# Optimization experiments

Hardware: AMD Instinct MI355X
Metric: run time of the kernel (lower is better)

Reference implementation:

```python
import jax, jax.numpy as jnp
import numpy as np

# static config (matches init_kwargs)
B, HID, NH, D = 1, 1024, 16, 64
T, Hh, W = 8, 32, 32
TT, TH, TW = 2, 8, 8            # tile sizes (numel 128)
WT, WH, WW = 6 // TT, 16 // TH, 16 // TW  # window in tiles: 3,2,2
NTT, NTH, NTW = T // TT, Hh // TH, W // TW  # 4,4,4
NTILE = NTT * NTH * NTW          # 64
TILE = TT * TH * TW              # 128
WK = WT * WH * WW                # 12 kv tiles per q tile
S = T * Hh * W


def _dim_window(nt, w):
    left = w // 2
    right = w // 2 + (w % 2) - 1
    center = jnp.clip(jnp.arange(nt), left, nt - 1 - right)
    return center[:, None] - left + jnp.arange(w)  # [nt, w]


def _kv_tile_idx():
    kt = _dim_window(NTT, WT)  # [NTT, WT]
    kh = _dim_window(NTH, WH)  # [NTH, WH]
    kw = _dim_window(NTW, WW)  # [NTW, WW]
    idx = (kt[:, None, None, :, None, None] * (NTH * NTW)
           + kh[None, :, None, None, :, None] * NTW
           + kw[None, None, :, None, None, :])
    return idx.reshape(NTILE, WK)


def _to_tiles(x, nh):
    # [B, S, nh*D] -> [B, nh, NTILE, TILE, D]; seq laid out (ntt tt nth th ntw tw)
    x = x.reshape(B, NTT, TT, NTH, TH, NTW, TW, nh, D)
    x = x.transpose(0, 7, 1, 3, 5, 2, 4, 6, 8)
    return x.reshape(B, nh, NTILE, TILE, D)


def _from_tiles(o):
    # [B, NH, NTILE, TILE, D] -> [B, S, NH*D]
    o = o.reshape(B, NH, NTT, NTH, NTW, TT, TH, TW, D)
    o = o.transpose(0, 2, 5, 3, 6, 4, 7, 1, 8)
    return o.reshape(B, S, NH * D)


def setup_inputs() -> dict:
    key = jax.random.key(0)
    ks = jax.random.split(key, 5)
    sc = 1.0 / np.sqrt(HID)
    return {
        'hidden_states': jax.random.normal(ks[0], (B, S, HID), jnp.float32),
        'wq': jax.random.normal(ks[1], (HID, NH * D), jnp.float32) * sc,
        'wk': jax.random.normal(ks[2], (HID, NH * D), jnp.float32) * sc,
        'wv': jax.random.normal(ks[3], (HID, NH * D), jnp.float32) * sc,
        'wo': jax.random.normal(ks[4], (NH * D, HID), jnp.float32) * sc,
    }


def reference(hidden_states, wq, wk, wv, wo):
    kv_idx = _kv_tile_idx()  # [NTILE, WK]
    q = _to_tiles(hidden_states @ wq, NH)  # [B,NH,NTILE,TILE,D]
    k = _to_tiles(hidden_states @ wk, NH)
    v = _to_tiles(hidden_states @ wv, NH)
    # gather each query tile's exact kv window (mask fully satisfied by construction)
    kg = k[:, :, kv_idx].reshape(B, NH, NTILE, WK * TILE, D)
    vg = v[:, :, kv_idx].reshape(B, NH, NTILE, WK * TILE, D)
    scores = jnp.einsum('bhnqd,bhnkd->bhnqk', q, kg) * (1.0 / np.sqrt(D))
    p = jax.nn.softmax(scores, axis=-1)
    o = jnp.einsum('bhnqk,bhnkd->bhnqd', p, vg)
    return _from_tiles(o) @ wo
```

## Files before the change

kernel.cpp:

```cpp
#include <hip/hip_runtime.h>
#include <hip/hip_bf16.h>
#include <math.h>

typedef __attribute__((ext_vector_type(8))) short          short8;
typedef __attribute__((ext_vector_type(8))) unsigned short u16x8;
typedef __attribute__((ext_vector_type(2))) unsigned int   u32x2;
typedef __attribute__((ext_vector_type(4))) float          f32x4;

#define MFMA_BF16(a, b, c) __builtin_amdgcn_mfma_f32_16x16x32_bf16((a), (b), (c), 0, 0, 0)

#define GLOAD_LDS16(gp, lp)                                        \
  __builtin_amdgcn_global_load_lds(                                \
      (const __attribute__((address_space(1))) void*)(gp),         \
      (__attribute__((address_space(3))) void*)(lp), 16, 0, 0)


__device__ __forceinline__ unsigned short f2bf(float f) {
  union { float f; unsigned int u; } v; v.f = f;
  unsigned int r = v.u + 0x7fffu + ((v.u >> 16) & 1u);
  return (unsigned short)(r >> 16);
}
__device__ __forceinline__ unsigned int pack2bf(float a, float b) {
  union { float f; unsigned int u; } x, y; x.f = a; y.f = b;
  return ((x.u + 0x8000u) >> 16) | ((y.u + 0x8000u) & 0xffff0000u);
}

__device__ __forceinline__ int row_to_seq(int r) {
  int tile = r >> 7, pos = r & 127;
  int ntt = tile >> 4, nth = (tile >> 2) & 3, ntw = tile & 3;
  int tt  = pos >> 6,  th  = (pos >> 3) & 7,  tw  = pos & 7;
  return ((ntt * 2 + tt) << 10) | ((nth * 8 + th) << 5) | (ntw * 8 + tw);
}

__global__ __launch_bounds__(256) void permute_hs(const float* __restrict__ in,
                                                  unsigned short* __restrict__ out) {
  int cid = blockIdx.x * 256 + threadIdx.x;
  int r = cid >> 7, c = (cid & 127) * 8;
  int s = row_to_seq(r);
  const float* f = in + (size_t)s * 1024 + c;
  u16x8 v;
#pragma unroll
  for (int j = 0; j < 8; ++j) v[j] = f2bf(f[j]);
  *(u16x8*)(out + (size_t)r * 1024 + c) = v;
}

__global__ __launch_bounds__(256) void transpose_w(const float* __restrict__ w0,
                                                   const float* __restrict__ w1,
                                                   const float* __restrict__ w2,
                                                   const float* __restrict__ w3,
                                                   unsigned short* __restrict__ out) {
  __shared__ unsigned short Lt[64 * 68];
  int m = blockIdx.y;
  const float* W = (m == 0) ? w0 : (m == 1) ? w1 : (m == 2) ? w2 : w3;
  unsigned short* O = out + (size_t)m * 1048576;
  int k0 = (blockIdx.x >> 4) * 64, n0 = (blockIdx.x & 15) * 64;
  int tid = threadIdx.x;
#pragma unroll
  for (int i = 0; i < 2; ++i) {
    int cid = i * 256 + tid;
    int kr = cid >> 3, c = cid & 7;
    const float* f = W + (size_t)(k0 + kr) * 1024 + n0 + c * 8;
#pragma unroll
    for (int j = 0; j < 8; ++j) Lt[(c * 8 + j) * 68 + kr] = f2bf(f[j]);
  }
  __syncthreads();
#pragma unroll
  for (int i = 0; i < 2; ++i) {
    int cid = i * 256 + tid;
    int nr = cid >> 3, c = cid & 7;
    u16x8 v;
#pragma unroll
    for (int j = 0; j < 8; ++j) v[j] = Lt[nr * 68 + c * 8 + j];
    *(u16x8*)(O + (size_t)(n0 + nr) * 1024 + k0 + c * 8) = v;
  }
}

template <int SCATTER, int OUT_F32>
__device__ __forceinline__ void gemm_bt_body(const unsigned short* __restrict__ A,
                                             const unsigned short* __restrict__ Bt,
                                             void* __restrict__ Cv,
                                             int row0, int col0, float scale) {
  __shared__ unsigned short As[128 * 64];
  __shared__ unsigned short Bs[128 * 64];
  const int tid  = threadIdx.x;
  const int lane = tid & 63, w = tid >> 6;
  const int quad = lane >> 4, lm = lane & 15;
  const int wr = (w >> 1) * 64, wc = (w & 1) * 64;
  f32x4 acc[4][4] = {};
  for (int kt = 0; kt < 16; ++kt) {
    const int k0 = kt * 64;
    __syncthreads();
#pragma unroll
    for (int i = 0; i < 4; ++i) {
      int cid = i * 256 + tid;
      int r = cid >> 3, c = cid & 7;
      int cg = c ^ (r & 7);
      int base = (i * 256 + (tid & 192)) * 8;
      GLOAD_LDS16(A  + (size_t)(row0 + r) * 1024 + k0 + cg * 8, As + base);
      GLOAD_LDS16(Bt + (size_t)(col0 + r) * 1024 + k0 + cg * 8, Bs + base);
    }
    __syncthreads();
#pragma unroll
    for (int kh = 0; kh < 2; ++kh) {
      short8 af[4], bf[4];
#pragma unroll
      for (int t = 0; t < 4; ++t) {
        int ca = (kh * 4 + quad) ^ (lm & 7);
        af[t] = *(const short8*)(As + (wr + t * 16 + lm) * 64 + ca * 8);
        bf[t] = *(const short8*)(Bs + (wc + t * 16 + lm) * 64 + ca * 8);
      }
#pragma unroll
      for (int rt = 0; rt < 4; ++rt)
#pragma unroll
        for (int ct = 0; ct < 4; ++ct)
          acc[rt][ct] = MFMA_BF16(af[rt], bf[ct], acc[rt][ct]);
    }
  }
#pragma unroll
  for (int rt = 0; rt < 4; ++rt)
#pragma unroll
    for (int ct = 0; ct < 4; ++ct)
#pragma unroll
      for (int g = 0; g < 4; ++g) {
        int R  = row0 + wr + rt * 16 + quad * 4 + g;
        int Cc = col0 + wc + ct * 16 + lm;
        int Rs = SCATTER ? row_to_seq(R) : R;
        float vv = acc[rt][ct][g] * scale;
        if (OUT_F32) ((float*)Cv)[(size_t)Rs * 1024 + Cc] = vv;
        else ((unsigned short*)Cv)[(size_t)Rs * 1024 + Cc] = f2bf(vv);
      }
}

__global__ __launch_bounds__(256) void gemm_qkv(const unsigned short* __restrict__ A,
                                                const unsigned short* __restrict__ Wt,
                                                unsigned short* __restrict__ QKV) {
  float scale = (blockIdx.z == 0) ? 0.18033688011112042f : 1.0f;
  gemm_bt_body<0, 0>(A, Wt + (size_t)blockIdx.z * 1048576,
                     QKV + (size_t)blockIdx.z * 8388608,
                     blockIdx.y * 128, blockIdx.x * 128, scale);
}

__global__ __launch_bounds__(256) void gemm_out(const unsigned short* __restrict__ A,
                                                const unsigned short* __restrict__ Wt,
                                                float* __restrict__ Cout) {
  gemm_bt_body<1, 1>(A, Wt, Cout, blockIdx.y * 128, blockIdx.x * 128, 1.0f);
}

__global__ __launch_bounds__(256) void transpose_v(const unsigned short* __restrict__ V,
                                                   unsigned short* __restrict__ Vt) {
  __shared__ unsigned short Lt[64 * 136];
  int kt = blockIdx.x, h = blockIdx.y, tid = threadIdx.x;
#pragma unroll
  for (int i = 0; i < 4; ++i) {
    int cid = i * 256 + tid;
    int r = cid >> 3, c = cid & 7;
    u16x8 v = *(const u16x8*)(V + (size_t)(kt * 128 + r) * 1024 + h * 64 + c * 8);
#pragma unroll
    for (int j = 0; j < 8; ++j) Lt[(c * 8 + j) * 136 + r] = v[j];
  }
  __syncthreads();
#pragma unroll
  for (int i = 0; i < 4; ++i) {
    int cid = i * 256 + tid;
    int d = cid >> 4, c = cid & 15;
    u16x8 v = *(const u16x8*)(Lt + d * 136 + c * 8);
    *(u16x8*)(Vt + (size_t)(h * 64 + d) * 8192 + kt * 128 + c * 8) = v;
  }
}

__global__ __launch_bounds__(512, 4) void attn(const unsigned short* __restrict__ Q,
                                               const unsigned short* __restrict__ K,
                                               const unsigned short* __restrict__ Vt,
                                               unsigned short* __restrict__ O) {
  __shared__ unsigned short Ks[128 * 64];
  __shared__ unsigned short Vs[64 * 128];
  __shared__ unsigned short Pb[8 * 16 * 64];

  const int tid  = threadIdx.x;
  const int lane = tid & 63, w = tid >> 6;
  const int quad = lane >> 4, lm = lane & 15;
  unsigned short* Pbw = Pb + w * 1024;

  const int h = blockIdx.x >> 6, qt = blockIdx.x & 63;
  const int ntt = qt >> 4, nth = (qt >> 2) & 3, ntw = qt & 3;
  const int kt0 = min(max(ntt, 1), 2) - 1;
  const int kh0 = min(max(nth, 1), 3) - 1;
  const int kw0 = min(max(ntw, 1), 3) - 1;

  short8 bq[2];
#pragma unroll
  for (int kh = 0; kh < 2; ++kh)
    bq[kh] = *(const short8*)(Q + (size_t)(qt * 128 + w * 16 + lm) * 1024
                                + h * 64 + kh * 32 + quad * 8);

  short8 ones8;
#pragma unroll
  for (int j = 0; j < 8; ++j) ones8[j] = (short)0x3F80;

  f32x4 o_acc[4] = {};
  f32x4 l_acc = {};

  {
    const int kvt0 = kt0 * 16 + kh0 * 4 + kw0;
#pragma unroll
    for (int i = 0; i < 2; ++i) {
      int cid = i * 512 + tid;
      int r = cid >> 3, c = cid & 7, cg = c ^ (r & 7);
      int base = (i * 512 + (tid & 448)) * 8;
      GLOAD_LDS16(K + (size_t)(kvt0 * 128 + r) * 1024 + h * 64 + cg * 8, Ks + base);
    }
  }
  __syncthreads();

  for (int it = 0; it < 12; ++it) {
    const int tt2 = it >> 2, hh2 = (it >> 1) & 1, ww2 = it & 1;
    const int kvt = (kt0 + tt2) * 16 + (kh0 + hh2) * 4 + (kw0 + ww2);

#pragma unroll
    for (int i = 0; i < 2; ++i) {
      int cid = i * 512 + tid;
      int d = cid >> 4, c = cid & 15, cg = c ^ (d & 7);
      int base = (i * 512 + (tid & 448)) * 8;
      GLOAD_LDS16(Vt + (size_t)(h * 64 + d) * 8192 + kvt * 128 + cg * 8, Vs + base);
    }

    f32x4 sa[8] = {};
#pragma unroll
    for (int kh = 0; kh < 2; ++kh) {
      short8 ak[8];
#pragma unroll
      for (int rt = 0; rt < 8; ++rt)
        ak[rt] = *(const short8*)(Ks + (rt * 16 + lm) * 64 + (((kh * 4 + quad) ^ (lm & 7)) * 8));
#pragma unroll
      for (int rt = 0; rt < 8; ++rt)
        sa[rt] = MFMA_BF16(ak[rt], bq[kh], sa[rt]);
    }

    u32x2 pk[8];
#pragma unroll
    for (int rt = 0; rt < 8; ++rt) {
      pk[rt][0] = pack2bf(exp2f(sa[rt][0]), exp2f(sa[rt][1]));
      pk[rt][1] = pack2bf(exp2f(sa[rt][2]), exp2f(sa[rt][3]));
    }

    __syncthreads();

    if (it < 11) {
      const int jt = it + 1;
      const int t2 = jt >> 2, h2 = (jt >> 1) & 1, w2 = jt & 1;
      const int kvn = (kt0 + t2) * 16 + (kh0 + h2) * 4 + (kw0 + w2);
#pragma unroll
      for (int i = 0; i < 2; ++i) {
        int cid = i * 512 + tid;
        int r = cid >> 3, c = cid & 7, cg = c ^ (r & 7);
        int base = (i * 512 + (tid & 448)) * 8;
        GLOAD_LDS16(K + (size_t)(kvn * 128 + r) * 1024 + h * 64 + cg * 8, Ks + base);
      }
    }

#pragma unroll
    for (int half = 0; half < 2; ++half) {
#pragma unroll
      for (int rt4 = 0; rt4 < 4; ++rt4) {
        *(u32x2*)(Pbw + lm * 64 + (((rt4 * 2 + (quad >> 1)) ^ (lm & 7)) * 8) + (quad & 1) * 4)
            = pk[half * 4 + rt4];
      }
#pragma unroll
      for (int ks2 = 0; ks2 < 2; ++ks2) {
        short8 ap = *(const short8*)(Pbw + lm * 64 + (((ks2 * 4 + quad) ^ (lm & 7)) * 8));
        l_acc = MFMA_BF16(ap, ones8, l_acc);
        const int ks = half * 2 + ks2;
#pragma unroll
        for (int nt = 0; nt < 4; ++nt) {
          short8 bv = *(const short8*)(Vs + (nt * 16 + lm) * 128 + (((ks * 4 + quad) ^ (lm & 7)) * 8));
          o_acc[nt] = MFMA_BF16(ap, bv, o_acc[nt]);
        }
      }
    }

    __syncthreads();
  }

#pragma unroll
  for (int g = 0; g < 4; ++g) {
    float inv = 1.0f / l_acc[g];
#pragma unroll
    for (int nt = 0; nt < 4; ++nt) {
      int R = qt * 128 + w * 16 + quad * 4 + g;
      O[(size_t)R * 1024 + h * 64 + nt * 16 + lm] = f2bf(o_acc[nt][g] * inv);
    }
  }
}

extern "C" void kernel_launch(void* const* d_in, const int* in_sizes, int n_in,
                              void* d_out, int out_size, void* d_ws, size_t ws_size,
                              hipStream_t stream) {
  const float* hs = (const float*)d_in[0];
  const float* wq = (const float*)d_in[1];
  const float* wk = (const float*)d_in[2];
  const float* wv = (const float*)d_in[3];
  const float* wo = (const float*)d_in[4];
  float* out = (float*)d_out;

  const size_t NEL = 8388608;
  unsigned short* ws  = (unsigned short*)d_ws;
  unsigned short* HSt = ws;
  unsigned short* Qb  = ws + 1 * NEL;
  unsigned short* Kb  = ws + 2 * NEL;
  unsigned short* Vb  = ws + 3 * NEL;
  unsigned short* Vtb = ws + 4 * NEL;
  unsigned short* Ot  = ws + 5 * NEL;
  unsigned short* Wt  = ws + 6 * NEL;
  if (ws_size < (6 * NEL + 4 * 1048576) * sizeof(unsigned short)) return;

  permute_hs<<<4096, 256, 0, stream>>>(hs, HSt);
  transpose_w<<<dim3(256, 4), 256, 0, stream>>>(wq, wk, wv, wo, Wt);
  gemm_qkv<<<dim3(8, 64, 3), 256, 0, stream>>>(HSt, Wt, Qb);
  transpose_v<<<dim3(64, 16), 256, 0, stream>>>(Vb, Vtb);
  attn<<<1024, 512, 0, stream>>>(Qb, Kb, Vtb, Ot);
  gemm_out<<<dim3(8, 64, 1), 256, 0, stream>>>(Ot, Wt + 3 * 1048576, out);
  (void)in_sizes; (void)n_in; (void)out_size;
}
```

Before: 293.1 us.

## Pair query tiles sharing a KV window per attention block

Each attention block now handles two query tiles that are adjacent in time and therefore share the same 12-tile KV window. Every K/V tile loaded into LDS is reused for both, which halves global KV traffic and the number of blocks. The kernel also raises wave priority around MFMA groups and packs bf16 pairs with a single perm instruction. The cost is more registers for two accumulator sets, a doubled P buffer, and only 512 blocks, which lowers occupancy and parallelism.

```diff
diff --git a/kernel.cpp b/kernel.cpp
--- a/kernel.cpp
+++ b/kernel.cpp
@@ -22,7 +22,7 @@
 }
 __device__ __forceinline__ unsigned int pack2bf(float a, float b) {
   union { float f; unsigned int u; } x, y; x.f = a; y.f = b;
-  return ((x.u + 0x8000u) >> 16) | ((y.u + 0x8000u) & 0xffff0000u);
+  return __builtin_amdgcn_perm(y.u + 0x8000u, x.u + 0x8000u, 0x07060302u);
 }
 
 __device__ __forceinline__ int row_to_seq(int r) {
@@ -174,31 +174,38 @@
                                                unsigned short* __restrict__ O) {
   __shared__ unsigned short Ks[128 * 64];
   __shared__ unsigned short Vs[64 * 128];
-  __shared__ unsigned short Pb[8 * 16 * 64];
+  __shared__ unsigned short Pb[2 * 8 * 16 * 64];
 
   const int tid  = threadIdx.x;
   const int lane = tid & 63, w = tid >> 6;
   const int quad = lane >> 4, lm = lane & 15;
-  unsigned short* Pbw = Pb + w * 1024;
-
-  const int h = blockIdx.x >> 6, qt = blockIdx.x & 63;
-  const int ntt = qt >> 4, nth = (qt >> 2) & 3, ntw = qt & 3;
-  const int kt0 = min(max(ntt, 1), 2) - 1;
+  unsigned short* PbA = Pb + w * 1024;
+  unsigned short* PbB = Pb + 8192 + w * 1024;
+
+  const int h = blockIdx.x >> 5, pr = blockIdx.x & 31;
+  const int pt = pr >> 4, rem = pr & 15;
+  const int nth = rem >> 2, ntw = rem & 3;
+  const int qtA = pt * 32 + nth * 4 + ntw;
+  const int qtB = qtA + 16;
+  const int kt0 = pt;
   const int kh0 = min(max(nth, 1), 3) - 1;
   const int kw0 = min(max(ntw, 1), 3) - 1;
 
-  short8 bq[2];
-#pragma unroll
-  for (int kh = 0; kh < 2; ++kh)
-    bq[kh] = *(const short8*)(Q + (size_t)(qt * 128 + w * 16 + lm) * 1024
-                                + h * 64 + kh * 32 + quad * 8);
+  short8 bqA[2], bqB[2];
+#pragma unroll
+  for (int kh = 0; kh < 2; ++kh) {
+    bqA[kh] = *(const short8*)(Q + (size_t)(qtA * 128 + w * 16 + lm) * 1024
+                                 + h * 64 + kh * 32 + quad * 8);
+    bqB[kh] = *(const short8*)(Q + (size_t)(qtB * 128 + w * 16 + lm) * 1024
+                                 + h * 64 + kh * 32 + quad * 8);
+  }
 
   short8 ones8;
 #pragma unroll
   for (int j = 0; j < 8; ++j) ones8[j] = (short)0x3F80;
 
-  f32x4 o_acc[4] = {};
-  f32x4 l_acc = {};
+  f32x4 oA[4] = {}, oB[4] = {};
+  f32x4 lA = {}, lB = {};
 
   {
     const int kvt0 = kt0 * 16 + kh0 * 4 + kw0;
@@ -224,23 +231,46 @@
       GLOAD_LDS16(Vt + (size_t)(h * 64 + d) * 8192 + kvt * 128 + cg * 8, Vs + base);
     }
 
-    f32x4 sa[8] = {};
-#pragma unroll
-    for (int kh = 0; kh < 2; ++kh) {
-      short8 ak[8];
-#pragma unroll
-      for (int rt = 0; rt < 8; ++rt)
-        ak[rt] = *(const short8*)(Ks + (rt * 16 + lm) * 64 + (((kh * 4 + quad) ^ (lm & 7)) * 8));
-#pragma unroll
-      for (int rt = 0; rt < 8; ++rt)
-        sa[rt] = MFMA_BF16(ak[rt], bq[kh], sa[rt]);
-    }
-
-    u32x2 pk[8];
-#pragma unroll
-    for (int rt = 0; rt < 8; ++rt) {
-      pk[rt][0] = pack2bf(exp2f(sa[rt][0]), exp2f(sa[rt][1]));
-      pk[rt][1] = pack2bf(exp2f(sa[rt][2]), exp2f(sa[rt][3]));
+    u32x2 pkA[8], pkB[8];
+    {
+      f32x4 sa[8] = {};
+#pragma unroll
+      for (int kh = 0; kh < 2; ++kh) {
+        short8 ak[8];
+#pragma unroll
+        for (int rt = 0; rt < 8; ++rt)
+          ak[rt] = *(const short8*)(Ks + (rt * 16 + lm) * 64 + (((kh * 4 + quad) ^ (lm & 7)) * 8));
+        __builtin_amdgcn_s_setprio(1);
+#pragma unroll
+        for (int rt = 0; rt < 8; ++rt)
+          sa[rt] = MFMA_BF16(ak[rt], bqA[kh], sa[rt]);
+        __builtin_amdgcn_s_setprio(0);
+      }
+#pragma unroll
+      for (int rt = 0; rt < 8; ++rt) {
+        pkA[rt][0] = pack2bf(exp2f(sa[rt][0]), exp2f(sa[rt][1]));
+        pkA[rt][1] = pack2bf(exp2f(sa[rt][2]), exp2f(sa[rt][3]));
+      }
+    }
+    {
+      f32x4 sb[8] = {};
+#pragma unroll
+      for (int kh = 0; kh < 2; ++kh) {
+        short8 ak[8];
+#pragma unroll
+        for (int rt = 0; rt < 8; ++rt)
+          ak[rt] = *(const short8*)(Ks + (rt * 16 + lm) * 64 + (((kh * 4 + quad) ^ (lm & 7)) * 8));
+        __builtin_amdgcn_s_setprio(1);
+#pragma unroll
+        for (int rt = 0; rt < 8; ++rt)
+          sb[rt] = MFMA_BF16(ak[rt], bqB[kh], sb[rt]);
+        __builtin_amdgcn_s_setprio(0);
+      }
+#pragma unroll
+      for (int rt = 0; rt < 8; ++rt) {
+        pkB[rt][0] = pack2bf(exp2f(sb[rt][0]), exp2f(sb[rt][1]));
+        pkB[rt][1] = pack2bf(exp2f(sb[rt][2]), exp2f(sb[rt][3]));
+      }
     }
 
     __syncthreads();
@@ -262,18 +292,27 @@
     for (int half = 0; half < 2; ++half) {
 #pragma unroll
       for (int rt4 = 0; rt4 < 4; ++rt4) {
-        *(u32x2*)(Pbw + lm * 64 + (((rt4 * 2 + (quad >> 1)) ^ (lm & 7)) * 8) + (quad & 1) * 4)
-            = pk[half * 4 + rt4];
+        int off = lm * 64 + (((rt4 * 2 + (quad >> 1)) ^ (lm & 7)) * 8) + (quad & 1) * 4;
+        *(u32x2*)(PbA + off) = pkA[half * 4 + rt4];
+        *(u32x2*)(PbB + off) = pkB[half * 4 + rt4];
       }
 #pragma unroll
       for (int ks2 = 0; ks2 < 2; ++ks2) {
-        short8 ap = *(const short8*)(Pbw + lm * 64 + (((ks2 * 4 + quad) ^ (lm & 7)) * 8));
-        l_acc = MFMA_BF16(ap, ones8, l_acc);
+        int aoff = lm * 64 + (((ks2 * 4 + quad) ^ (lm & 7)) * 8);
+        short8 apA = *(const short8*)(PbA + aoff);
+        short8 apB = *(const short8*)(PbB + aoff);
+        __builtin_amdgcn_s_setprio(1);
+        lA = MFMA_BF16(apA, ones8, lA);
+        lB = MFMA_BF16(apB, ones8, lB);
+        __builtin_amdgcn_s_setprio(0);
         const int ks = half * 2 + ks2;
 #pragma unroll
         for (int nt = 0; nt < 4; ++nt) {
           short8 bv = *(const short8*)(Vs + (nt * 16 + lm) * 128 + (((ks * 4 + quad) ^ (lm & 7)) * 8));
-          o_acc[nt] = MFMA_BF16(ap, bv, o_acc[nt]);
+          __builtin_amdgcn_s_setprio(1);
+          oA[nt] = MFMA_BF16(apA, bv, oA[nt]);
+          oB[nt] = MFMA_BF16(apB, bv, oB[nt]);
+          __builtin_amdgcn_s_setprio(0);
         }
       }
     }
@@ -283,11 +322,14 @@
 
 #pragma unroll
   for (int g = 0; g < 4; ++g) {
-    float inv = 1.0f / l_acc[g];
+    float invA = 1.0f / lA[g];
+    float invB = 1.0f / lB[g];
 #pragma unroll
     for (int nt = 0; nt < 4; ++nt) {
-      int R = qt * 128 + w * 16 + quad * 4 + g;
-      O[(size_t)R * 1024 + h * 64 + nt * 16 + lm] = f2bf(o_acc[nt][g] * inv);
+      int RA = qtA * 128 + w * 16 + quad * 4 + g;
+      int RB = qtB * 128 + w * 16 + quad * 4 + g;
+      O[(size_t)RA * 1024 + h * 64 + nt * 16 + lm] = f2bf(oA[nt][g] * invA);
+      O[(size_t)RB * 1024 + h * 64 + nt * 16 + lm] = f2bf(oB[nt][g] * invB);
     }
   }
 }
@@ -317,7 +359,7 @@
   transpose_w<<<dim3(256, 4), 256, 0, stream>>>(wq, wk, wv, wo, Wt);
   gemm_qkv<<<dim3(8, 64, 3), 256, 0, stream>>>(HSt, Wt, Qb);
   transpose_v<<<dim3(64, 16), 256, 0, stream>>>(Vb, Vtb);
-  attn<<<1024, 512, 0, stream>>>(Qb, Kb, Vtb, Ot);
+  attn<<<512, 512, 0, stream>>>(Qb, Kb, Vtb, Ot);
   gemm_out<<<dim3(8, 64, 1), 256, 0, stream>>>(Ot, Wt + 3 * 1048576, out);
   (void)in_sizes; (void)n_in; (void)out_size;
 }
```

New measurement: 458.7 us. 56.5% more time.
